# Optimization experiments

Measured on AMD Instinct MI355X. Metric: run time of the kernel, lower is better.

## Reference

```python
import jax, jax.numpy as jnp
import numpy as np

RADIUS = 3
T_STEPS = 2
NEG = -9.0e8
B, L, DEG = 256, 64, 6
FEAT, BOND, FP, OUT = 39, 10, 256, 1


def _leaky(x):
    return jax.nn.leaky_relu(x, 0.01)


def _gru(x, h, wih, whh, bih, bhh):
    # PyTorch GRUCell: gates ordered (r, z, n)
    gi = x @ wih.T + bih
    gh = h @ whh.T + bhh
    ir, iz, inn = jnp.split(gi, 3, axis=-1)
    hr, hz, hn = jnp.split(gh, 3, axis=-1)
    r = jax.nn.sigmoid(ir + hr)
    z = jax.nn.sigmoid(iz + hz)
    n = jnp.tanh(inn + r * hn)
    return (1.0 - z) * n + z * h


def _forward(atom_list, bond_list, atom_mask,
             atom_fc_w, atom_fc_b, neighbor_fc_w, neighbor_fc_b,
             align_w, align_b, attend_w, attend_b,
             gru_wih, gru_whh, gru_bih, gru_bhh,
             mol_align_w, mol_align_b, mol_attend_w, mol_attend_b,
             mol_gru_wih, mol_gru_whh, mol_gru_bih, mol_gru_bhh,
             out_w, out_b,
             atom_degree_list, bond_degree_list):
    b, l, _ = atom_list.shape
    mask = atom_mask[..., None]                                   # [B,L,1]
    atom_feature = _leaky(atom_list @ atom_fc_w.T + atom_fc_b)    # [B,L,FP]

    # per-molecule neighbor gather (padding index = L-1)
    bidx = jnp.arange(b)[:, None, None]
    atom_nb = atom_list[bidx, atom_degree_list]                    # [B,L,deg,FEAT]
    bond_nb = bond_list[bidx, bond_degree_list]                    # [B,L,deg,BOND]
    neighbor_feature = _leaky(
        jnp.concatenate([atom_nb, bond_nb], axis=-1) @ neighbor_fc_w.T + neighbor_fc_b
    )                                                              # [B,L,deg,FP]

    attend_mask = (atom_degree_list != l - 1).astype(atom_feature.dtype)[..., None]
    softmax_mask = jnp.where(atom_degree_list == l - 1, NEG, 0.0).astype(atom_feature.dtype)[..., None]

    for d in range(RADIUS):
        af_exp = jnp.broadcast_to(atom_feature[:, :, None, :], neighbor_feature.shape)
        feature_align = jnp.concatenate([af_exp, neighbor_feature], axis=-1)  # [B,L,deg,2FP]
        align_score = _leaky(feature_align @ align_w[d].T + align_b[d]) + softmax_mask
        attention_weight = jax.nn.softmax(align_score, axis=-2) * attend_mask
        attended = neighbor_feature @ attend_w[d].T + attend_b[d]
        context = jax.nn.elu(jnp.sum(attention_weight * attended, axis=-2))   # [B,L,FP]
        atom_feature = _gru(context.reshape(b * l, -1), atom_feature.reshape(b * l, -1),
                            gru_wih[d], gru_whh[d], gru_bih[d], gru_bhh[d]).reshape(b, l, -1)
        # faithful to original: self-feature broadcast across neighbor dim
        neighbor_feature = jnp.broadcast_to(jax.nn.relu(atom_feature)[:, :, None, :],
                                            neighbor_feature.shape)

    mol_feature = jnp.sum(jax.nn.relu(atom_feature) * mask, axis=-2)          # [B,FP]
    mol_softmax_mask = jnp.where(atom_mask == 0, NEG, 0.0).astype(atom_feature.dtype)[..., None]

    for _ in range(T_STEPS):
        m_exp = jnp.broadcast_to(mol_feature[:, None, :], atom_feature.shape)
        mol_align = jnp.concatenate([m_exp, atom_feature], axis=-1)           # [B,L,2FP]
        mol_score = _leaky(mol_align @ mol_align_w.T + mol_align_b) + mol_softmax_mask
        mol_w = jax.nn.softmax(mol_score, axis=-2) * mask
        attended = atom_feature @ mol_attend_w.T + mol_attend_b
        mol_context = jax.nn.elu(jnp.sum(mol_w * attended, axis=-2))
        mol_feature = _gru(mol_context, mol_feature,
                           mol_gru_wih, mol_gru_whh, mol_gru_bih, mol_gru_bhh)

    mol_prediction = mol_feature @ out_w.T + out_b
    return atom_feature, mol_prediction


def setup_inputs() -> dict:
    key = jax.random.key(0)
    ks = jax.random.split(key, 20)
    s = 0.05
    return {
        "atom_list": jax.random.normal(ks[0], (B, L, FEAT), jnp.float32),
        "bond_list": jax.random.normal(ks[1], (B, L, BOND), jnp.float32),
        "atom_degree_list": jax.random.randint(ks[2], (B, L, DEG), 0, L),
        "bond_degree_list": jax.random.randint(ks[3], (B, L, DEG), 0, L),
        "atom_mask": jnp.ones((B, L), jnp.float32),
        "atom_fc_w": jax.random.normal(ks[4], (FP, FEAT)) * s,
        "atom_fc_b": jnp.zeros((FP,)),
        "neighbor_fc_w": jax.random.normal(ks[5], (FP, FEAT + BOND)) * s,
        "neighbor_fc_b": jnp.zeros((FP,)),
        "align_w": jax.random.normal(ks[6], (RADIUS, 1, 2 * FP)) * s,
        "align_b": jnp.zeros((RADIUS, 1)),
        "attend_w": jax.random.normal(ks[7], (RADIUS, FP, FP)) * s,
        "attend_b": jnp.zeros((RADIUS, FP)),
        "gru_wih": jax.random.normal(ks[8], (RADIUS, 3 * FP, FP)) * s,
        "gru_whh": jax.random.normal(ks[9], (RADIUS, 3 * FP, FP)) * s,
        "gru_bih": jnp.zeros((RADIUS, 3 * FP)),
        "gru_bhh": jnp.zeros((RADIUS, 3 * FP)),
        "mol_align_w": jax.random.normal(ks[10], (1, 2 * FP)) * s,
        "mol_align_b": jnp.zeros((1,)),
        "mol_attend_w": jax.random.normal(ks[11], (FP, FP)) * s,
        "mol_attend_b": jnp.zeros((FP,)),
        "mol_gru_wih": jax.random.normal(ks[12], (3 * FP, FP)) * s,
        "mol_gru_whh": jax.random.normal(ks[13], (3 * FP, FP)) * s,
        "mol_gru_bih": jnp.zeros((3 * FP,)),
        "mol_gru_bhh": jnp.zeros((3 * FP,)),
        "out_w": jax.random.normal(ks[14], (OUT, FP)) * s,
        "out_b": jnp.zeros((OUT,)),
    }


def reference(atom_list, bond_list, atom_degree_list, bond_degree_list, atom_mask,
              atom_fc_w, atom_fc_b, neighbor_fc_w, neighbor_fc_b,
              align_w, align_b, attend_w, attend_b,
              gru_wih, gru_whh, gru_bih, gru_bhh,
              mol_align_w, mol_align_b, mol_attend_w, mol_attend_b,
              mol_gru_wih, mol_gru_whh, mol_gru_bih, mol_gru_bhh,
              out_w, out_b):
    return _forward(atom_list, bond_list, atom_mask,
                    atom_fc_w, atom_fc_b, neighbor_fc_w, neighbor_fc_b,
                    align_w, align_b, attend_w, attend_b,
                    gru_wih, gru_whh, gru_bih, gru_bhh,
                    mol_align_w, mol_align_b, mol_attend_w, mol_attend_b,
                    mol_gru_wih, mol_gru_whh, mol_gru_bih, mol_gru_bhh,
                    out_w, out_b,
                    atom_degree_list, bond_degree_list)
```

## Files before the change

### kernel.cpp

```cpp
#include <hip/hip_runtime.h>
#include <hip/hip_bf16.h>

#define NB 256
#define NL 64
#define DEG 6
#define FEAT 39
#define BOND 10
#define FP 256
#define NEGV (-9.0e8f)

using s16x8 = __attribute__((ext_vector_type(8))) short;
using f32x4 = __attribute__((ext_vector_type(4))) float;

__device__ __forceinline__ unsigned short f2bf(float f){
  unsigned u = __float_as_uint(f);
  u += 0x7fffu + ((u >> 16) & 1u);
  return (unsigned short)(u >> 16);
}
__device__ __forceinline__ float lo16(unsigned u){ return __uint_as_float(u << 16); }
__device__ __forceinline__ float hi16(unsigned u){ return __uint_as_float(u & 0xffff0000u); }

__device__ __forceinline__ float block_sum256(float v, float* scr){
  #pragma unroll
  for(int o=32;o>0;o>>=1) v += __shfl_down(v, o, 64);
  __syncthreads();
  if((threadIdx.x & 63) == 0) scr[threadIdx.x >> 6] = v;
  __syncthreads();
  return scr[0] + scr[1] + scr[2] + scr[3];
}
__device__ __forceinline__ float wave_allsum(float v){
  #pragma unroll
  for(int o=1;o<64;o<<=1) v += __shfl_xor(v, o, 64);
  return v;
}

#define MCVT_N0 65536
#define MCVT_N1 196608
#define MCVT_N2 196608
#define MCVT_TOT (MCVT_N0+MCVT_N1+MCVT_N2)
#define CTXPK_N (3*8*8192)
#define GPK_N   (3*2*8*24576)

__global__ void k_cvt_mol(const float* __restrict__ a0, const float* __restrict__ a1,
                          const float* __restrict__ a2, unsigned short* __restrict__ dst){
  int i = blockIdx.x*256 + threadIdx.x;
  if(i >= MCVT_TOT) return;
  int off = i; const float* src;
  if(off < MCVT_N0) src = a0;
  else { off -= MCVT_N0;
    if(off < MCVT_N1) src = a1;
    else { off -= MCVT_N1; src = a2; } }
  dst[i] = f2bf(src[off]);
}

__global__ void k_pack(const float* __restrict__ attend_w, const float* __restrict__ gru_wih,
                       const float* __restrict__ gru_whh,
                       unsigned short* __restrict__ ctx_pk, unsigned short* __restrict__ gates_pk){
  int i = blockIdx.x*256 + threadIdx.x;
  if(i < CTXPK_N){
    int d = i >> 16;
    int rem = i & 65535;
    int kk = rem >> 13;
    int r2 = rem & 8191;
    int g = r2 >> 9;
    int l = (r2 >> 3) & 63;
    int q = r2 & 7;
    int row = g*16 + (l & 15);
    int k = kk*32 + (l >> 4)*8 + q;
    ctx_pk[i] = f2bf(attend_w[((size_t)d*256 + row)*256 + k]);
  } else {
    int j = i - CTXPK_N;
    if(j >= GPK_N) return;
    int d = j / 393216;
    int rem = j - d*393216;
    int nc = rem / 196608; rem -= nc*196608;
    int kk = rem / 24576;  rem -= kk*24576;
    int f = rem >> 9;
    int l = (rem >> 3) & 63;
    int q = rem & 7;
    int s = f >> 3, g = f & 7;
    int row = nc*128 + g*16 + (l & 15);
    int k = kk*32 + (l >> 4)*8 + q;
    float v = (s < 3) ? gru_wih[(((size_t)d*3 + s)*256 + row)*256 + k]
                      : gru_whh[(((size_t)d*3 + (s-3))*256 + row)*256 + k];
    gates_pk[j] = f2bf(v);
  }
}

__global__ void k_tr(const float* __restrict__ aw, const float* __restrict__ nw,
                     float* __restrict__ afcT, unsigned short* __restrict__ nfcT){
  int i = blockIdx.x*256 + threadIdx.x;
  if(i < 40*256){
    int k = i >> 8, r = i & 255;
    afcT[i] = (k < FEAT) ? aw[r*FEAT + k] : 0.f;
  } else {
    int j = i - 40*256;
    int k = j >> 8, r = j & 255;
    nfcT[j] = (k < FEAT+BOND) ? f2bf(nw[r*(FEAT+BOND) + k]) : (unsigned short)0;
  }
}

__global__ __launch_bounds__(256) void k_atom4(const float* __restrict__ atom,
    const float* __restrict__ afcT, const float* __restrict__ bias, float* __restrict__ af){
  __shared__ float x_s[4][40];
  const int t = threadIdx.x, bl0 = blockIdx.x*4;
  for(int idx=t; idx<4*FEAT; idx+=256){ int a=idx/FEAT, k=idx%FEAT; x_s[a][k]=atom[(bl0+a)*FEAT+k]; }
  if(t < 4) x_s[t][39] = 0.f;
  __syncthreads();
  const int w = t>>6, t0 = (t&63)*4, row = bl0 + w;
  float4 b4 = *(const float4*)&bias[t0];
  float acc[4] = {b4.x, b4.y, b4.z, b4.w};
  for(int k=0;k<40;++k){
    float iv = x_s[w][k];
    float4 wv = *(const float4*)&afcT[(k<<8)+t0];
    acc[0]=fmaf(iv,wv.x,acc[0]); acc[1]=fmaf(iv,wv.y,acc[1]);
    acc[2]=fmaf(iv,wv.z,acc[2]); acc[3]=fmaf(iv,wv.w,acc[3]);
  }
  float4 o;
  o.x = acc[0]>0.f?acc[0]:0.01f*acc[0]; o.y = acc[1]>0.f?acc[1]:0.01f*acc[1];
  o.z = acc[2]>0.f?acc[2]:0.01f*acc[2]; o.w = acc[3]>0.f?acc[3]:0.01f*acc[3];
  *(float4*)&af[(size_t)row*FP + t0] = o;
}

__global__ __launch_bounds__(256) void k_nbr4(const float* __restrict__ atom,
    const float* __restrict__ bond, const int* __restrict__ adl, const int* __restrict__ bdl,
    const unsigned short* __restrict__ nfcT, const float* __restrict__ bn,
    const float* __restrict__ alw, const float* __restrict__ alb,
    const float* __restrict__ af, float* __restrict__ wnf, float* __restrict__ swb){
  __shared__ float in_s[4][DEG][52];
  __shared__ int   ai_s[4][DEG];
  const int t = threadIdx.x, bl0 = blockIdx.x*4;
  if(t < 24){ int a=t/6, d=t%6; ai_s[a][d] = adl[(bl0+a)*DEG + d]; }
  __syncthreads();
  for(int idx=t; idx<4*DEG*(FEAT+BOND); idx+=256){
    int a = idx/(DEG*(FEAT+BOND)), rem = idx%(DEG*(FEAT+BOND));
    int d = rem/(FEAT+BOND), k = rem%(FEAT+BOND);
    int bb = (bl0+a) >> 6;
    float v;
    if(k < FEAT) v = atom[((size_t)bb*NL + ai_s[a][d])*FEAT + k];
    else { int bi = bdl[(bl0+a)*DEG + d]; v = bond[((size_t)bb*NL + bi)*BOND + (k-FEAT)]; }
    in_s[a][d][k] = v;
  }
  if(t < 24){ int a=t/6, d=t%6; in_s[a][d][49]=0.f; in_s[a][d][50]=0.f; in_s[a][d][51]=0.f; }
  __syncthreads();
  const int w = t>>6, lane = t&63, t0 = lane*4, row = bl0 + w;
  float acc[DEG][4] = {};
  for(int k=0;k<52;++k){
    uint2 u = *(const uint2*)&nfcT[(k<<8) + t0];
    float w0=lo16(u.x), w1=hi16(u.x), w2=lo16(u.y), w3=hi16(u.y);
    #pragma unroll
    for(int d=0;d<DEG;++d){
      float iv = in_s[w][d][k];
      acc[d][0]=fmaf(iv,w0,acc[d][0]); acc[d][1]=fmaf(iv,w1,acc[d][1]);
      acc[d][2]=fmaf(iv,w2,acc[d][2]); acc[d][3]=fmaf(iv,w3,acc[d][3]);
    }
  }
  float4 bnv = *(const float4*)&bn[t0];
  float bna[4] = {bnv.x, bnv.y, bnv.z, bnv.w};
  float nf[DEG][4];
  #pragma unroll
  for(int d=0;d<DEG;++d)
    #pragma unroll
    for(int j=0;j<4;++j){ float v = acc[d][j] + bna[j]; nf[d][j] = v>0.f ? v : 0.01f*v; }
  float4 af4 = *(const float4*)&af[(size_t)row*FP + t0];
  float4 a1  = *(const float4*)&alw[t0];
  float4 a2  = *(const float4*)&alw[FP + t0];
  float sa = wave_allsum(af4.x*a1.x + af4.y*a1.y + af4.z*a1.z + af4.w*a1.w);
  float sd[DEG];
  #pragma unroll
  for(int d=0;d<DEG;++d)
    sd[d] = wave_allsum(nf[d][0]*a2.x + nf[d][1]*a2.y + nf[d][2]*a2.z + nf[d][3]*a2.w);
  float ab = alb[0];
  float sc[DEG], msk[DEG];
  #pragma unroll
  for(int d=0;d<DEG;++d){
    float v = sa + sd[d] + ab;
    v = v>0.f ? v : 0.01f*v;
    msk[d] = (ai_s[w][d] == NL-1) ? 0.f : 1.f;
    sc[d] = v + (msk[d] > 0.f ? 0.f : NEGV);
  }
  float m = sc[0];
  #pragma unroll
  for(int d=1;d<DEG;++d) m = fmaxf(m, sc[d]);
  float e[DEG], Z = 0.f;
  #pragma unroll
  for(int d=0;d<DEG;++d){ e[d] = expf(sc[d]-m); Z += e[d]; }
  float wgt[DEG], sw = 0.f;
  #pragma unroll
  for(int d=0;d<DEG;++d){ wgt[d] = e[d]/Z*msk[d]; sw += wgt[d]; }
  float o[4] = {};
  #pragma unroll
  for(int d=0;d<DEG;++d)
    #pragma unroll
    for(int j=0;j<4;++j) o[j] = fmaf(wgt[d], nf[d][j], o[j]);
  float4 ov; ov.x=o[0]; ov.y=o[1]; ov.z=o[2]; ov.w=o[3];
  *(float4*)&wnf[(size_t)row*FP + t0] = ov;
  if(lane == 0) swb[row] = sw;
}

__global__ __launch_bounds__(512) void k_radius4(
    const float* __restrict__ wnf, float* __restrict__ af, const float* __restrict__ swb,
    const unsigned short* __restrict__ ctx_pk, const unsigned short* __restrict__ gates_pk,
    const float* __restrict__ attend_b,
    const float* __restrict__ gru_bih, const float* __restrict__ gru_bhh){
  __shared__ __align__(16) unsigned short Cf[32*512];
  const int t = threadIdx.x;
  const int w = t>>6, lane = t&63, lr = lane&15, ks = lane>>4;
  const int wm = w>>2, wn = w&3;
  const int m0 = blockIdx.x*64;

  for(int d=0; d<3; ++d){
    const float* bat  = attend_b + d*256;
    const float* bihd = gru_bih + d*768;
    const float* bhhd = gru_bhh + d*768;

    __syncthreads();
    f32x4 acc2[2][4] = {};
    #pragma unroll
    for(int kk=0; kk<8; ++kk){
      const unsigned short* ct = ctx_pk + ((size_t)d*8 + kk)*8192;
      s16x8 xf[2];
      #pragma unroll
      for(int mf=0; mf<2; ++mf){
        int row = m0 + wm*32 + mf*16 + lr;
        float4 v0, v1;
        if(d == 0){
          const float* sp = wnf + (size_t)row*256 + kk*32 + ks*8;
          v0 = *(const float4*)sp; v1 = *(const float4*)(sp+4);
        } else {
          const float* sp = af + (size_t)row*256 + kk*32 + ks*8;
          v0 = *(const float4*)sp; v1 = *(const float4*)(sp+4);
          float sw = swb[row];
          v0.x=fmaxf(v0.x,0.f)*sw; v0.y=fmaxf(v0.y,0.f)*sw;
          v0.z=fmaxf(v0.z,0.f)*sw; v0.w=fmaxf(v0.w,0.f)*sw;
          v1.x=fmaxf(v1.x,0.f)*sw; v1.y=fmaxf(v1.y,0.f)*sw;
          v1.z=fmaxf(v1.z,0.f)*sw; v1.w=fmaxf(v1.w,0.f)*sw;
        }
        unsigned short tmp[8] = {f2bf(v0.x),f2bf(v0.y),f2bf(v0.z),f2bf(v0.w),
                                 f2bf(v1.x),f2bf(v1.y),f2bf(v1.z),f2bf(v1.w)};
        xf[mf] = *(s16x8*)tmp;
      }
      #pragma unroll
      for(int nf=0; nf<4; ++nf){
        s16x8 wf = *(const s16x8*)(ct + ((wn*4 + nf)*64 + lane)*8);
        acc2[0][nf] = __builtin_amdgcn_mfma_f32_16x16x32_bf16(wf, xf[0], acc2[0][nf],0,0,0);
        acc2[1][nf] = __builtin_amdgcn_mfma_f32_16x16x32_bf16(wf, xf[1], acc2[1][nf],0,0,0);
      }
    }
    #pragma unroll
    for(int mf=0; mf<2; ++mf){
      float swv = swb[m0 + wm*32 + mf*16 + lr];
      #pragma unroll
      for(int nf=0; nf<4; ++nf){
        int nb = wn*64 + nf*16 + ks*4;
        float4 b4 = *(const float4*)&bat[nb];
        float bj[4] = {b4.x, b4.y, b4.z, b4.w};
        unsigned short o4[4];
        #pragma unroll
        for(int j=0;j<4;++j){
          float v = acc2[mf][nf][j] + swv*bj[j];
          v = v > 0.f ? v : expm1f(v);
          o4[j] = f2bf(v);
        }
        int gm = wm*2 + mf;
        int kkp = wn*2 + (nf>>1);
        int lhi = ((nf & 1) << 1) | (ks >> 1);
        int addr = (gm*8 + kkp)*512 + (lhi*16 + lr)*8 + (ks & 1)*4;
        *(uint2*)&Cf[addr] = *(uint2*)o4;
      }
    }
    __syncthreads();
    float hnew0[2][2][4];
    float hnew1[2][2][4];
    for(int nc=0; nc<2; ++nc){
      f32x4 aR[2][2] = {}, aZ[2][2] = {}, aN[2][2] = {}, aH[2][2] = {};
      #pragma unroll
      for(int kk=0; kk<8; ++kk){
        const unsigned short* gp = gates_pk + ((size_t)(d*2 + nc)*8 + kk)*24576;
        s16x8 hf[2];
        #pragma unroll
        for(int mf=0; mf<2; ++mf){
          int row = m0 + wm*32 + mf*16 + lr;
          const float* sp = af + (size_t)row*256 + kk*32 + ks*8;
          float4 v0 = *(const float4*)sp, v1 = *(const float4*)(sp+4);
          unsigned short tmp[8] = {f2bf(v0.x),f2bf(v0.y),f2bf(v0.z),f2bf(v0.w),
                                   f2bf(v1.x),f2bf(v1.y),f2bf(v1.z),f2bf(v1.w)};
          hf[mf] = *(s16x8*)tmp;
        }
        s16x8 cf0 = *(const s16x8*)&Cf[((wm*2 + 0)*8 + kk)*512 + lane*8];
        s16x8 cf1 = *(const s16x8*)&Cf[((wm*2 + 1)*8 + kk)*512 + lane*8];
        #pragma unroll
        for(int fn=0; fn<2; ++fn){
          int g = wn*2 + fn;
          s16x8 b0 = *(const s16x8*)(gp + ((0*8 + g)*64 + lane)*8);
          s16x8 b1 = *(const s16x8*)(gp + ((1*8 + g)*64 + lane)*8);
          s16x8 b2 = *(const s16x8*)(gp + ((2*8 + g)*64 + lane)*8);
          s16x8 b3 = *(const s16x8*)(gp + ((3*8 + g)*64 + lane)*8);
          s16x8 b4 = *(const s16x8*)(gp + ((4*8 + g)*64 + lane)*8);
          s16x8 b5 = *(const s16x8*)(gp + ((5*8 + g)*64 + lane)*8);
          aR[0][fn] = __builtin_amdgcn_mfma_f32_16x16x32_bf16(cf0, b0, aR[0][fn],0,0,0);
          aR[1][fn] = __builtin_amdgcn_mfma_f32_16x16x32_bf16(cf1, b0, aR[1][fn],0,0,0);
          aZ[0][fn] = __builtin_amdgcn_mfma_f32_16x16x32_bf16(cf0, b1, aZ[0][fn],0,0,0);
          aZ[1][fn] = __builtin_amdgcn_mfma_f32_16x16x32_bf16(cf1, b1, aZ[1][fn],0,0,0);
          aN[0][fn] = __builtin_amdgcn_mfma_f32_16x16x32_bf16(cf0, b2, aN[0][fn],0,0,0);
          aN[1][fn] = __builtin_amdgcn_mfma_f32_16x16x32_bf16(cf1, b2, aN[1][fn],0,0,0);
          aR[0][fn] = __builtin_amdgcn_mfma_f32_16x16x32_bf16(hf[0], b3, aR[0][fn],0,0,0);
          aR[1][fn] = __builtin_amdgcn_mfma_f32_16x16x32_bf16(hf[1], b3, aR[1][fn],0,0,0);
          aZ[0][fn] = __builtin_amdgcn_mfma_f32_16x16x32_bf16(hf[0], b4, aZ[0][fn],0,0,0);
          aZ[1][fn] = __builtin_amdgcn_mfma_f32_16x16x32_bf16(hf[1], b4, aZ[1][fn],0,0,0);
          aH[0][fn] = __builtin_amdgcn_mfma_f32_16x16x32_bf16(hf[0], b5, aH[0][fn],0,0,0);
          aH[1][fn] = __builtin_amdgcn_mfma_f32_16x16x32_bf16(hf[1], b5, aH[1][fn],0,0,0);
        }
      }
      float (*hn_)[2][4] = (nc == 0) ? hnew0 : hnew1;
      int nbase = nc*128;
      #pragma unroll
      for(int mf=0; mf<2; ++mf)
        #pragma unroll
        for(int fn=0; fn<2; ++fn){
          int n = nbase + wn*32 + fn*16 + lr;
          float brz = bihd[n] + bhhd[n];
          float bzz = bihd[256+n] + bhhd[256+n];
          float bnn = bihd[512+n];
          float bhn = bhhd[512+n];
          #pragma unroll
          for(int j=0;j<4;++j){
            int m = m0 + wm*32 + mf*16 + ks*4 + j;
            float hold = af[(size_t)m*256 + n];
            float r = 1.f/(1.f + expf(-(aR[mf][fn][j] + brz)));
            float z = 1.f/(1.f + expf(-(aZ[mf][fn][j] + bzz)));
            float ng = tanhf(aN[mf][fn][j] + bnn + r*(aH[mf][fn][j] + bhn));
            hn_[mf][fn][j] = (1.f - z)*ng + z*hold;
          }
        }
    }
    __syncthreads();
    #pragma unroll
    for(int nc=0; nc<2; ++nc){
      float (*hn_)[2][4] = (nc == 0) ? hnew0 : hnew1;
      int nbase = nc*128;
      #pragma unroll
      for(int mf=0; mf<2; ++mf)
        #pragma unroll
        for(int fn=0; fn<2; ++fn){
          int n = nbase + wn*32 + fn*16 + lr;
          #pragma unroll
          for(int j=0;j<4;++j){
            int m = m0 + wm*32 + mf*16 + ks*4 + j;
            af[(size_t)m*256 + n] = hn_[mf][fn][j];
          }
        }
    }
  }
}

__global__ __launch_bounds__(256) void k_lin_gemm(
    const float* __restrict__ Xsrc, const unsigned short* __restrict__ Wbf,
    const float* __restrict__ bias, float* __restrict__ Y){
  __shared__ unsigned short A_lds[64][264];
  __shared__ unsigned short B_lds[64][264];
  const int t = threadIdx.x;
  const int m0 = (blockIdx.x >> 2) * 64, n0 = (blockIdx.x & 3) * 64;
  const int rb = t >> 4, cb = (t & 15) * 16;
  for(int i=0;i<4;++i){
    int row = i*16 + rb;
    const float* src = Xsrc + (size_t)(m0+row)*FP + cb;
    unsigned short tmp[16];
    #pragma unroll
    for(int q=0;q<4;++q){
      float4 v = ((const float4*)src)[q];
      tmp[q*4+0]=f2bf(v.x); tmp[q*4+1]=f2bf(v.y); tmp[q*4+2]=f2bf(v.z); tmp[q*4+3]=f2bf(v.w);
    }
    *(s16x8*)&A_lds[row][cb]   = *(s16x8*)&tmp[0];
    *(s16x8*)&A_lds[row][cb+8] = *(s16x8*)&tmp[8];
    const unsigned short* wsrc = Wbf + (size_t)(n0+row)*FP + cb;
    *(s16x8*)&B_lds[row][cb]   = *(const s16x8*)&wsrc[0];
    *(s16x8*)&B_lds[row][cb+8] = *(const s16x8*)&wsrc[8];
  }
  __syncthreads();
  const int w = t>>6, lane = t&63, lr = lane&15, ks = lane>>4;
  const int wr = (w>>1)*32, wc = (w&1)*32;
  f32x4 acc[2][2] = {};
  #pragma unroll
  for(int kk=0;kk<8;++kk){
    int ko = kk*32 + ks*8;
    s16x8 a0 = *(const s16x8*)&A_lds[wr+lr][ko];
    s16x8 a1 = *(const s16x8*)&A_lds[wr+16+lr][ko];
    s16x8 b0 = *(const s16x8*)&B_lds[wc+lr][ko];
    s16x8 b1 = *(const s16x8*)&B_lds[wc+16+lr][ko];
    acc[0][0] = __builtin_amdgcn_mfma_f32_16x16x32_bf16(a0,b0,acc[0][0],0,0,0);
    acc[0][1] = __builtin_amdgcn_mfma_f32_16x16x32_bf16(a0,b1,acc[0][1],0,0,0);
    acc[1][0] = __builtin_amdgcn_mfma_f32_16x16x32_bf16(a1,b0,acc[1][0],0,0,0);
    acc[1][1] = __builtin_amdgcn_mfma_f32_16x16x32_bf16(a1,b1,acc[1][1],0,0,0);
  }
  #pragma unroll
  for(int fm=0;fm<2;++fm)
    #pragma unroll
    for(int fn=0;fn<2;++fn){
      int n = n0 + wc + fn*16 + lr;
      float bv = bias[n];
      #pragma unroll
      for(int j=0;j<4;++j){
        int m = m0 + wr + fm*16 + ks*4 + j;
        Y[(size_t)m*FP + n] = acc[fm][fn][j] + bv;
      }
    }
}

__global__ __launch_bounds__(256) void k_gates32(
    const unsigned short* __restrict__ ctxbf, const float* __restrict__ h_glob,
    const unsigned short* __restrict__ wihbf, const unsigned short* __restrict__ whhbf,
    const float* __restrict__ bih, const float* __restrict__ bhh,
    float* __restrict__ h_out){
  __shared__ unsigned short A_ctx[32][40];
  __shared__ unsigned short A_h[32][40];
  __shared__ unsigned short B_lds[6][64][40];
  const int t = threadIdx.x;
  const int m0 = (blockIdx.x >> 2) * 32, nc = (blockIdx.x & 3) * 64;
  const int w = t>>6, lane = t&63, lr = lane&15, ks = lane>>4;
  const int mh = (w>>1)*16, nh = (w&1)*32;
  f32x4 acc[6][2] = {};
  for(int kk=0;kk<8;++kk){
    const int k0 = kk*32;
    __syncthreads();
    {
      int row = t>>3, c4 = (t&7)*4;
      *(uint2*)&A_ctx[row][c4] = *(const uint2*)(ctxbf + (size_t)(m0+row)*FP + k0 + c4);
      float4 hv = *(const float4*)(h_glob + (size_t)(m0+row)*FP + k0 + c4);
      unsigned short ht[4] = {f2bf(hv.x), f2bf(hv.y), f2bf(hv.z), f2bf(hv.w)};
      *(uint2*)&A_h[row][c4] = *(uint2*)ht;
    }
    #pragma unroll
    for(int i=0;i<6;++i){
      int idx = i*256 + t;
      int s = idx >> 8, rem = idx & 255;
      int row = rem >> 2, c8 = (rem & 3)*8;
      const unsigned short* wsrc = (s < 3)
          ? wihbf + (size_t)(s*FP + nc + row)*FP + k0 + c8
          : whhbf + (size_t)((s-3)*FP + nc + row)*FP + k0 + c8;
      *(s16x8*)&B_lds[s][row][c8] = *(const s16x8*)wsrc;
    }
    __syncthreads();
    s16x8 ac = *(const s16x8*)&A_ctx[mh+lr][ks*8];
    s16x8 ah = *(const s16x8*)&A_h[mh+lr][ks*8];
    #pragma unroll
    for(int s=0;s<6;++s){
      s16x8 a = (s < 3) ? ac : ah;
      #pragma unroll
      for(int fn=0;fn<2;++fn){
        s16x8 b = *(const s16x8*)&B_lds[s][nh+fn*16+lr][ks*8];
        acc[s][fn] = __builtin_amdgcn_mfma_f32_16x16x32_bf16(a,b,acc[s][fn],0,0,0);
      }
    }
  }
  #pragma unroll
  for(int fn=0;fn<2;++fn){
    int n = nc + nh + fn*16 + lr;
    float bir = bih[n], biz = bih[FP+n], bin_ = bih[2*FP+n];
    float bhr = bhh[n], bhz = bhh[FP+n], bhn  = bhh[2*FP+n];
    #pragma unroll
    for(int j=0;j<4;++j){
      int m = m0 + mh + ks*4 + j;
      float h = h_glob[(size_t)m*FP + n];
      float ir = acc[0][fn][j]+bir, iz = acc[1][fn][j]+biz, inn = acc[2][fn][j]+bin_;
      float hr = acc[3][fn][j]+bhr, hz = acc[4][fn][j]+bhz, hn  = acc[5][fn][j]+bhn;
      float r = 1.f/(1.f + expf(-(ir+hr)));
      float z = 1.f/(1.f + expf(-(iz+hz)));
      float ng = tanhf(inn + r*hn);
      h_out[(size_t)m*FP + n] = (1.f-z)*ng + z*h;
    }
  }
}

__global__ void k_finalize(const float* __restrict__ af, const float* __restrict__ mask,
                           float* __restrict__ molfeat, float* __restrict__ out_af){
  const int b = blockIdx.x, t = threadIdx.x;
  __shared__ float msk_s[NL];
  if(t < NL) msk_s[t] = mask[b*NL + t];
  __syncthreads();
  float mf = 0.f;
  for(int l=0;l<NL;++l){
    float v = af[(size_t)(b*NL + l)*FP + t];
    out_af[(size_t)(b*NL + l)*FP + t] = v;
    mf = fmaf(fmaxf(v,0.f), msk_s[l], mf);
  }
  molfeat[b*FP + t] = mf;
}

__global__ void k_mol_ctx(const float* __restrict__ af, const float* __restrict__ att,
    const float* __restrict__ mfin, const float* __restrict__ maw,
    const float* __restrict__ mabp, const float* __restrict__ mask,
    unsigned short* __restrict__ ctxb){
  const int b = blockIdx.x, t = threadIdx.x;
  __shared__ float mf_s[FP];
  __shared__ float sc_s[NL], aw_s[NL], scr[4];
  mf_s[t] = mfin[b*FP + t];
  __syncthreads();
  float sa = block_sum256(maw[t]*mf_s[t], scr);
  int l = t >> 2, q = t & 3;
  float p = 0.f;
  {
    const float4* ar = (const float4*)(af + (size_t)(b*NL + l)*FP + q*64);
    const float4* w2 = (const float4*)(maw + FP + q*64);
    #pragma unroll
    for(int k=0;k<16;++k){
      float4 a = ar[k], ww = w2[k];
      p = fmaf(a.x,ww.x,p); p = fmaf(a.y,ww.y,p);
      p = fmaf(a.z,ww.z,p); p = fmaf(a.w,ww.w,p);
    }
  }
  p += __shfl_xor(p, 1, 64);
  p += __shfl_xor(p, 2, 64);
  if(q == 0){
    float mv = mask[b*NL + l];
    float v = sa + p + mabp[0];
    v = v > 0.f ? v : 0.01f*v;
    sc_s[l] = v + (mv == 0.f ? NEGV : 0.f);
  }
  __syncthreads();
  if(t < NL){
    float s = sc_s[t];
    float m = s;
    #pragma unroll
    for(int o=32;o>0;o>>=1) m = fmaxf(m, __shfl_xor(m, o, 64));
    float e = expf(s - m);
    float Z = e;
    #pragma unroll
    for(int o=32;o>0;o>>=1) Z += __shfl_xor(Z, o, 64);
    aw_s[t] = e / Z * mask[b*NL + t];
  }
  __syncthreads();
  float acc = 0.f;
  for(int l2=0;l2<NL;++l2) acc = fmaf(aw_s[l2], att[(size_t)(b*NL + l2)*FP + t], acc);
  float c = acc > 0.f ? acc : expm1f(acc);
  ctxb[b*FP + t] = f2bf(c);
}

__global__ void k_out(const float* __restrict__ molfeat, const float* __restrict__ ow,
                      const float* __restrict__ ob, float* __restrict__ outp){
  const int b = blockIdx.x, t = threadIdx.x;
  __shared__ float scr[4];
  float s = block_sum256(molfeat[b*FP + t]*ow[t], scr);
  if(t == 0) outp[b] = s + ob[0];
}

extern "C" void kernel_launch(void* const* d_in, const int* in_sizes, int n_in,
                              void* d_out, int out_size, void* d_ws, size_t ws_size,
                              hipStream_t stream){
  const float* atom_list = (const float*)d_in[0];
  const float* bond_list = (const float*)d_in[1];
  const int*   adl       = (const int*)d_in[2];
  const int*   bdl       = (const int*)d_in[3];
  const float* amask     = (const float*)d_in[4];
  const float* afc_w     = (const float*)d_in[5];
  const float* afc_b     = (const float*)d_in[6];
  const float* nfc_w     = (const float*)d_in[7];
  const float* nfc_b     = (const float*)d_in[8];
  const float* align_w   = (const float*)d_in[9];
  const float* align_b   = (const float*)d_in[10];
  const float* attend_w  = (const float*)d_in[11];
  const float* attend_b  = (const float*)d_in[12];
  const float* gru_wih   = (const float*)d_in[13];
  const float* gru_whh   = (const float*)d_in[14];
  const float* gru_bih   = (const float*)d_in[15];
  const float* gru_bhh   = (const float*)d_in[16];
  const float* mol_align_w  = (const float*)d_in[17];
  const float* mol_align_b  = (const float*)d_in[18];
  const float* mol_attend_w = (const float*)d_in[19];
  const float* mol_attend_b = (const float*)d_in[20];
  const float* mg_wih    = (const float*)d_in[21];
  const float* mg_whh    = (const float*)d_in[22];
  const float* mg_bih    = (const float*)d_in[23];
  const float* mg_bhh    = (const float*)d_in[24];
  const float* out_w     = (const float*)d_in[25];
  const float* out_b     = (const float*)d_in[26];

  float* out_af   = (float*)d_out;
  float* out_pred = out_af + (size_t)NB*NL*FP;

  const size_t NROW = (size_t)NB*NL;
  const size_t F32_CNT = 2*NROW*FP + NROW + 2*(size_t)NB*FP + 40*256;
  const size_t U16_CNT = (size_t)NB*FP + MCVT_TOT + 52*256 + CTXPK_N + GPK_N;
  const size_t NEED = F32_CNT*4 + U16_CNT*2;

  if(ws_size >= NEED){
    float* af_a    = (float*)d_ws;
    float* wnf     = af_a + NROW*FP;
    float* swb     = wnf  + NROW*FP;
    float* mf_a    = swb  + NROW;
    float* mf_b    = mf_a + (size_t)NB*FP;
    float* afcT    = mf_b + (size_t)NB*FP;
    unsigned short* ctxbf_m = (unsigned short*)(afcT + 40*256);
    unsigned short* maw_bf  = ctxbf_m + (size_t)NB*FP;
    unsigned short* mgih_bf = maw_bf + MCVT_N0;
    unsigned short* mghh_bf = mgih_bf + MCVT_N1;
    unsigned short* nfcT_bf = mghh_bf + MCVT_N2;
    unsigned short* ctx_pk  = nfcT_bf + 52*256;
    unsigned short* gates_pk= ctx_pk + CTXPK_N;

    k_cvt_mol<<<(MCVT_TOT+255)/256, 256, 0, stream>>>(mol_attend_w, mg_wih, mg_whh, maw_bf);
    k_pack<<<(CTXPK_N+GPK_N)/256, 256, 0, stream>>>(attend_w, gru_wih, gru_whh, ctx_pk, gates_pk);
    k_tr<<<(40*256 + 52*256)/256, 256, 0, stream>>>(afc_w, nfc_w, afcT, nfcT_bf);

    k_atom4<<<NB*NL/4, 256, 0, stream>>>(atom_list, afcT, afc_b, af_a);
    k_nbr4<<<NB*NL/4, 256, 0, stream>>>(atom_list, bond_list, adl, bdl,
                                        nfcT_bf, nfc_b, align_w, align_b, af_a, wnf, swb);
    k_radius4<<<NB*NL/64, 512, 0, stream>>>(wnf, af_a, swb, ctx_pk, gates_pk,
                                            attend_b, gru_bih, gru_bhh);
    k_lin_gemm<<<(NB*NL/64)*4, 256, 0, stream>>>(af_a, maw_bf, mol_attend_b, wnf);
    k_finalize<<<NB, 256, 0, stream>>>(af_a, amask, mf_a, out_af);
    float* m_cur = mf_a; float* m_nxt = mf_b;
    for(int s=0; s<2; ++s){
      k_mol_ctx<<<NB, 256, 0, stream>>>(af_a, wnf, m_cur, mol_align_w, mol_align_b,
                                        amask, ctxbf_m);
      k_gates32<<<(NB/32)*4, 256, 0, stream>>>(ctxbf_m, m_cur, mgih_bf, mghh_bf,
                                               mg_bih, mg_bhh, m_nxt);
      float* tmp = m_cur; m_cur = m_nxt; m_nxt = tmp;
    }
    k_out<<<NB, 256, 0, stream>>>(m_cur, out_w, out_b, out_pred);
  } else {
    float* af = (float*)d_ws;
    k_atom4<<<NB*NL/4, 256, 0, stream>>>(atom_list, (const float*)afc_w, afc_b, af);
    (void)bond_list; (void)adl; (void)bdl; (void)amask;
    (void)align_w; (void)align_b; (void)attend_w; (void)attend_b;
    (void)gru_wih; (void)gru_whh; (void)gru_bih; (void)gru_bhh;
    (void)mol_align_w; (void)mol_align_b; (void)mol_attend_w; (void)mol_attend_b;
    (void)mg_wih; (void)mg_whh; (void)mg_bih; (void)mg_bhh; (void)out_w; (void)out_b;
  }
}
```

Baseline: 367.9 us.

## Stage radius weights through double-buffered LDS with register prefetch, halve row tile

The radius kernel now streams the attend and GRU weight tiles through a double-buffered shared-memory ring, prefetching the next tile into registers while the current one feeds the MFMAs. Previously every wave read its weights directly from global memory. The row tile per block shrinks from 64 to 32 and the GRU weight packing is re-laid out into 64-column chunks, so twice as many blocks launch with a min-blocks launch bound. This should hide weight-load latency and raise occupancy, at the cost of a barrier on every k-step and each block re-reading the full weight set for fewer rows.

```diff
diff --git a/kernel.cpp b/kernel.cpp
--- a/kernel.cpp
+++ b/kernel.cpp
@@ -38,8 +38,10 @@
 #define MCVT_N1 196608
 #define MCVT_N2 196608
 #define MCVT_TOT (MCVT_N0+MCVT_N1+MCVT_N2)
-#define CTXPK_N (3*8*8192)
-#define GPK_N   (3*2*8*24576)
+#define CT_U16 8192
+#define GT_U16 12288
+#define CTXPK_N (3*8*CT_U16)
+#define GPK_N   (3*4*8*GT_U16)
 
 __global__ void k_cvt_mol(const float* __restrict__ a0, const float* __restrict__ a1,
                           const float* __restrict__ a2, unsigned short* __restrict__ dst){
@@ -73,13 +75,13 @@
     if(j >= GPK_N) return;
     int d = j / 393216;
     int rem = j - d*393216;
-    int nc = rem / 196608; rem -= nc*196608;
-    int kk = rem / 24576;  rem -= kk*24576;
+    int nc = rem / 98304;  rem -= nc*98304;
+    int kk = rem / 12288;  rem -= kk*12288;
     int f = rem >> 9;
     int l = (rem >> 3) & 63;
     int q = rem & 7;
-    int s = f >> 3, g = f & 7;
-    int row = nc*128 + g*16 + (l & 15);
+    int s = f >> 2, gl = f & 3;
+    int row = nc*64 + gl*16 + (l & 15);
     int k = kk*32 + (l >> 4)*8 + q;
     float v = (s < 3) ? gru_wih[(((size_t)d*3 + s)*256 + row)*256 + k]
                       : gru_whh[(((size_t)d*3 + (s-3))*256 + row)*256 + k];
@@ -198,158 +200,148 @@
   if(lane == 0) swb[row] = sw;
 }
 
-__global__ __launch_bounds__(512) void k_radius4(
+__global__ __launch_bounds__(512, 4) void k_radius6(
     const float* __restrict__ wnf, float* __restrict__ af, const float* __restrict__ swb,
     const unsigned short* __restrict__ ctx_pk, const unsigned short* __restrict__ gates_pk,
     const float* __restrict__ attend_b,
     const float* __restrict__ gru_bih, const float* __restrict__ gru_bhh){
-  __shared__ __align__(16) unsigned short Cf[32*512];
+  __shared__ __align__(16) unsigned short Cf[2*8*512];
+  __shared__ __align__(16) unsigned short Bu[2][GT_U16];
   const int t = threadIdx.x;
   const int w = t>>6, lane = t&63, lr = lane&15, ks = lane>>4;
   const int wm = w>>2, wn = w&3;
-  const int m0 = blockIdx.x*64;
+  const int m0 = blockIdx.x*32;
+
+  s16x8 pf[3]; int pfn = 0;
+  auto LOADS = [&](int s){
+    if(s >= 120) return;
+    int d2 = s/40, r = s - d2*40;
+    const unsigned short* src; int n;
+    if(r < 8){ n = 2; src = ctx_pk + ((size_t)d2*8 + r)*CT_U16; }
+    else { int g = r - 8; n = 3; src = gates_pk + ((size_t)(d2*4 + (g>>3))*8 + (g&7))*GT_U16; }
+    pfn = n;
+    #pragma unroll
+    for(int c=0;c<3;++c) if(c < n) pf[c] = *(const s16x8*)(src + (w + c*8)*512 + lane*8);
+  };
+  auto WRITET = [&](int h){
+    #pragma unroll
+    for(int c=0;c<3;++c) if(c < pfn) *(s16x8*)&Bu[h][(w + c*8)*512 + lane*8] = pf[c];
+  };
+
+  LOADS(0);
+  WRITET(0);
+  LOADS(1);
+  int half = 0;
+  const float swv = swb[m0 + wm*16 + lr];
 
   for(int d=0; d<3; ++d){
     const float* bat  = attend_b + d*256;
     const float* bihd = gru_bih + d*768;
     const float* bhhd = gru_bhh + d*768;
-
-    __syncthreads();
-    f32x4 acc2[2][4] = {};
-    #pragma unroll
+    f32x4 acc2[4] = {};
     for(int kk=0; kk<8; ++kk){
-      const unsigned short* ct = ctx_pk + ((size_t)d*8 + kk)*8192;
-      s16x8 xf[2];
+      int s = d*40 + kk;
+      __syncthreads();
+      WRITET(half^1);
+      LOADS(s+2);
+      int row = m0 + wm*16 + lr;
+      float4 v0, v1;
+      if(d == 0){
+        const float* sp = wnf + (size_t)row*256 + kk*32 + ks*8;
+        v0 = *(const float4*)sp; v1 = *(const float4*)(sp+4);
+      } else {
+        const float* sp = af + (size_t)row*256 + kk*32 + ks*8;
+        v0 = *(const float4*)sp; v1 = *(const float4*)(sp+4);
+        v0.x=fmaxf(v0.x,0.f)*swv; v0.y=fmaxf(v0.y,0.f)*swv;
+        v0.z=fmaxf(v0.z,0.f)*swv; v0.w=fmaxf(v0.w,0.f)*swv;
+        v1.x=fmaxf(v1.x,0.f)*swv; v1.y=fmaxf(v1.y,0.f)*swv;
+        v1.z=fmaxf(v1.z,0.f)*swv; v1.w=fmaxf(v1.w,0.f)*swv;
+      }
+      unsigned short tmp[8] = {f2bf(v0.x),f2bf(v0.y),f2bf(v0.z),f2bf(v0.w),
+                               f2bf(v1.x),f2bf(v1.y),f2bf(v1.z),f2bf(v1.w)};
+      s16x8 xf = *(s16x8*)tmp;
       #pragma unroll
-      for(int mf=0; mf<2; ++mf){
-        int row = m0 + wm*32 + mf*16 + lr;
-        float4 v0, v1;
-        if(d == 0){
-          const float* sp = wnf + (size_t)row*256 + kk*32 + ks*8;
-          v0 = *(const float4*)sp; v1 = *(const float4*)(sp+4);
-        } else {
-          const float* sp = af + (size_t)row*256 + kk*32 + ks*8;
-          v0 = *(const float4*)sp; v1 = *(const float4*)(sp+4);
-          float sw = swb[row];
-          v0.x=fmaxf(v0.x,0.f)*sw; v0.y=fmaxf(v0.y,0.f)*sw;
-          v0.z=fmaxf(v0.z,0.f)*sw; v0.w=fmaxf(v0.w,0.f)*sw;
-          v1.x=fmaxf(v1.x,0.f)*sw; v1.y=fmaxf(v1.y,0.f)*sw;
-          v1.z=fmaxf(v1.z,0.f)*sw; v1.w=fmaxf(v1.w,0.f)*sw;
-        }
+      for(int nf=0; nf<4; ++nf){
+        s16x8 wf = *(const s16x8*)&Bu[half][((wn*4 + nf)*64 + lane)*8];
+        acc2[nf] = __builtin_amdgcn_mfma_f32_16x16x32_bf16(wf, xf, acc2[nf],0,0,0);
+      }
+      half ^= 1;
+    }
+    #pragma unroll
+    for(int nf=0; nf<4; ++nf){
+      int nb = wn*64 + nf*16 + ks*4;
+      float4 b4 = *(const float4*)&bat[nb];
+      float bj[4] = {b4.x, b4.y, b4.z, b4.w};
+      unsigned short o4[4];
+      #pragma unroll
+      for(int j=0;j<4;++j){
+        float v = acc2[nf][j] + swv*bj[j];
+        v = v > 0.f ? v : expm1f(v);
+        o4[j] = f2bf(v);
+      }
+      int gm = wm;
+      int kkp = wn*2 + (nf>>1);
+      int lhi = ((nf & 1) << 1) | (ks >> 1);
+      int addr = (gm*8 + kkp)*512 + (lhi*16 + lr)*8 + (ks & 1)*4;
+      *(uint2*)&Cf[addr] = *(uint2*)o4;
+    }
+    float hnew[4][4];
+    #pragma unroll
+    for(int nc=0; nc<4; ++nc){
+      f32x4 aR = {}, aZ = {}, aN = {}, aH = {};
+      #pragma unroll
+      for(int kk=0; kk<8; ++kk){
+        int s = d*40 + 8 + nc*8 + kk;
+        __syncthreads();
+        if(s < 119) WRITET(half^1);
+        LOADS(s+2);
+        int row = m0 + wm*16 + lr;
+        const float* sp = af + (size_t)row*256 + kk*32 + ks*8;
+        float4 v0 = *(const float4*)sp, v1 = *(const float4*)(sp+4);
         unsigned short tmp[8] = {f2bf(v0.x),f2bf(v0.y),f2bf(v0.z),f2bf(v0.w),
                                  f2bf(v1.x),f2bf(v1.y),f2bf(v1.z),f2bf(v1.w)};
-        xf[mf] = *(s16x8*)tmp;
-      }
-      #pragma unroll
-      for(int nf=0; nf<4; ++nf){
-        s16x8 wf = *(const s16x8*)(ct + ((wn*4 + nf)*64 + lane)*8);
-        acc2[0][nf] = __builtin_amdgcn_mfma_f32_16x16x32_bf16(wf, xf[0], acc2[0][nf],0,0,0);
-        acc2[1][nf] = __builtin_amdgcn_mfma_f32_16x16x32_bf16(wf, xf[1], acc2[1][nf],0,0,0);
-      }
-    }
-    #pragma unroll
-    for(int mf=0; mf<2; ++mf){
-      float swv = swb[m0 + wm*32 + mf*16 + lr];
-      #pragma unroll
-      for(int nf=0; nf<4; ++nf){
-        int nb = wn*64 + nf*16 + ks*4;
-        float4 b4 = *(const float4*)&bat[nb];
-        float bj[4] = {b4.x, b4.y, b4.z, b4.w};
-        unsigned short o4[4];
+        s16x8 hf = *(s16x8*)tmp;
+        s16x8 cf = *(const s16x8*)&Cf[(wm*8 + kk)*512 + lane*8];
+        s16x8 b0 = *(const s16x8*)&Bu[half][((0*4 + wn)*64 + lane)*8];
+        s16x8 b1 = *(const s16x8*)&Bu[half][((1*4 + wn)*64 + lane)*8];
+        s16x8 b2 = *(const s16x8*)&Bu[half][((2*4 + wn)*64 + lane)*8];
+        s16x8 b3 = *(const s16x8*)&Bu[half][((3*4 + wn)*64 + lane)*8];
+        s16x8 b4 = *(const s16x8*)&Bu[half][((4*4 + wn)*64 + lane)*8];
+        s16x8 b5 = *(const s16x8*)&Bu[half][((5*4 + wn)*64 + lane)*8];
+        aR = __builtin_amdgcn_mfma_f32_16x16x32_bf16(cf, b0, aR,0,0,0);
+        aZ = __builtin_amdgcn_mfma_f32_16x16x32_bf16(cf, b1, aZ,0,0,0);
+        aN = __builtin_amdgcn_mfma_f32_16x16x32_bf16(cf, b2, aN,0,0,0);
+        aR = __builtin_amdgcn_mfma_f32_16x16x32_bf16(hf, b3, aR,0,0,0);
+        aZ = __builtin_amdgcn_mfma_f32_16x16x32_bf16(hf, b4, aZ,0,0,0);
+        aH = __builtin_amdgcn_mfma_f32_16x16x32_bf16(hf, b5, aH,0,0,0);
+        half ^= 1;
+      }
+      {
+        int n = nc*64 + wn*16 + lr;
+        float brz = bihd[n] + bhhd[n];
+        float bzz = bihd[256+n] + bhhd[256+n];
+        float bnn = bihd[512+n];
+        float bhn = bhhd[512+n];
         #pragma unroll
         for(int j=0;j<4;++j){
-          float v = acc2[mf][nf][j] + swv*bj[j];
-          v = v > 0.f ? v : expm1f(v);
-          o4[j] = f2bf(v);
+          int m = m0 + wm*16 + ks*4 + j;
+          float hold = af[(size_t)m*256 + n];
+          float r = 1.f/(1.f + expf(-(aR[j] + brz)));
+          float z = 1.f/(1.f + expf(-(aZ[j] + bzz)));
+          float ng = tanhf(aN[j] + bnn + r*(aH[j] + bhn));
+          hnew[nc][j] = (1.f - z)*ng + z*hold;
         }
-        int gm = wm*2 + mf;
-        int kkp = wn*2 + (nf>>1);
-        int lhi = ((nf & 1) << 1) | (ks >> 1);
-        int addr = (gm*8 + kkp)*512 + (lhi*16 + lr)*8 + (ks & 1)*4;
-        *(uint2*)&Cf[addr] = *(uint2*)o4;
       }
     }
     __syncthreads();
-    float hnew0[2][2][4];
-    float hnew1[2][2][4];
-    for(int nc=0; nc<2; ++nc){
-      f32x4 aR[2][2] = {}, aZ[2][2] = {}, aN[2][2] = {}, aH[2][2] = {};
+    #pragma unroll
+    for(int nc=0; nc<4; ++nc){
+      int n = nc*64 + wn*16 + lr;
       #pragma unroll
-      for(int kk=0; kk<8; ++kk){
-        const unsigned short* gp = gates_pk + ((size_t)(d*2 + nc)*8 + kk)*24576;
-        s16x8 hf[2];
-        #pragma unroll
-        for(int mf=0; mf<2; ++mf){
-          int row = m0 + wm*32 + mf*16 + lr;
-          const float* sp = af + (size_t)row*256 + kk*32 + ks*8;
-          float4 v0 = *(const float4*)sp, v1 = *(const float4*)(sp+4);
-          unsigned short tmp[8] = {f2bf(v0.x),f2bf(v0.y),f2bf(v0.z),f2bf(v0.w),
-                                   f2bf(v1.x),f2bf(v1.y),f2bf(v1.z),f2bf(v1.w)};
-          hf[mf] = *(s16x8*)tmp;
-        }
-        s16x8 cf0 = *(const s16x8*)&Cf[((wm*2 + 0)*8 + kk)*512 + lane*8];
-        s16x8 cf1 = *(const s16x8*)&Cf[((wm*2 + 1)*8 + kk)*512 + lane*8];
-        #pragma unroll
-        for(int fn=0; fn<2; ++fn){
-          int g = wn*2 + fn;
-          s16x8 b0 = *(const s16x8*)(gp + ((0*8 + g)*64 + lane)*8);
-          s16x8 b1 = *(const s16x8*)(gp + ((1*8 + g)*64 + lane)*8);
-          s16x8 b2 = *(const s16x8*)(gp + ((2*8 + g)*64 + lane)*8);
-          s16x8 b3 = *(const s16x8*)(gp + ((3*8 + g)*64 + lane)*8);
-          s16x8 b4 = *(const s16x8*)(gp + ((4*8 + g)*64 + lane)*8);
-          s16x8 b5 = *(const s16x8*)(gp + ((5*8 + g)*64 + lane)*8);
-          aR[0][fn] = __builtin_amdgcn_mfma_f32_16x16x32_bf16(cf0, b0, aR[0][fn],0,0,0);
-          aR[1][fn] = __builtin_amdgcn_mfma_f32_16x16x32_bf16(cf1, b0, aR[1][fn],0,0,0);
-          aZ[0][fn] = __builtin_amdgcn_mfma_f32_16x16x32_bf16(cf0, b1, aZ[0][fn],0,0,0);
-          aZ[1][fn] = __builtin_amdgcn_mfma_f32_16x16x32_bf16(cf1, b1, aZ[1][fn],0,0,0);
-          aN[0][fn] = __builtin_amdgcn_mfma_f32_16x16x32_bf16(cf0, b2, aN[0][fn],0,0,0);
-          aN[1][fn] = __builtin_amdgcn_mfma_f32_16x16x32_bf16(cf1, b2, aN[1][fn],0,0,0);
-          aR[0][fn] = __builtin_amdgcn_mfma_f32_16x16x32_bf16(hf[0], b3, aR[0][fn],0,0,0);
-          aR[1][fn] = __builtin_amdgcn_mfma_f32_16x16x32_bf16(hf[1], b3, aR[1][fn],0,0,0);
-          aZ[0][fn] = __builtin_amdgcn_mfma_f32_16x16x32_bf16(hf[0], b4, aZ[0][fn],0,0,0);
-          aZ[1][fn] = __builtin_amdgcn_mfma_f32_16x16x32_bf16(hf[1], b4, aZ[1][fn],0,0,0);
-          aH[0][fn] = __builtin_amdgcn_mfma_f32_16x16x32_bf16(hf[0], b5, aH[0][fn],0,0,0);
-          aH[1][fn] = __builtin_amdgcn_mfma_f32_16x16x32_bf16(hf[1], b5, aH[1][fn],0,0,0);
-        }
-      }
-      float (*hn_)[2][4] = (nc == 0) ? hnew0 : hnew1;
-      int nbase = nc*128;
-      #pragma unroll
-      for(int mf=0; mf<2; ++mf)
-        #pragma unroll
-        for(int fn=0; fn<2; ++fn){
-          int n = nbase + wn*32 + fn*16 + lr;
-          float brz = bihd[n] + bhhd[n];
-          float bzz = bihd[256+n] + bhhd[256+n];
-          float bnn = bihd[512+n];
-          float bhn = bhhd[512+n];
-          #pragma unroll
-          for(int j=0;j<4;++j){
-            int m = m0 + wm*32 + mf*16 + ks*4 + j;
-            float hold = af[(size_t)m*256 + n];
-            float r = 1.f/(1.f + expf(-(aR[mf][fn][j] + brz)));
-            float z = 1.f/(1.f + expf(-(aZ[mf][fn][j] + bzz)));
-            float ng = tanhf(aN[mf][fn][j] + bnn + r*(aH[mf][fn][j] + bhn));
-            hn_[mf][fn][j] = (1.f - z)*ng + z*hold;
-          }
-        }
-    }
-    __syncthreads();
-    #pragma unroll
-    for(int nc=0; nc<2; ++nc){
-      float (*hn_)[2][4] = (nc == 0) ? hnew0 : hnew1;
-      int nbase = nc*128;
-      #pragma unroll
-      for(int mf=0; mf<2; ++mf)
-        #pragma unroll
-        for(int fn=0; fn<2; ++fn){
-          int n = nbase + wn*32 + fn*16 + lr;
-          #pragma unroll
-          for(int j=0;j<4;++j){
-            int m = m0 + wm*32 + mf*16 + ks*4 + j;
-            af[(size_t)m*256 + n] = hn_[mf][fn][j];
-          }
-        }
+      for(int j=0;j<4;++j){
+        int m = m0 + wm*16 + ks*4 + j;
+        af[(size_t)m*256 + n] = hnew[nc][j];
+      }
     }
   }
 }
@@ -605,7 +597,7 @@
     k_atom4<<<NB*NL/4, 256, 0, stream>>>(atom_list, afcT, afc_b, af_a);
     k_nbr4<<<NB*NL/4, 256, 0, stream>>>(atom_list, bond_list, adl, bdl,
                                         nfcT_bf, nfc_b, align_w, align_b, af_a, wnf, swb);
-    k_radius4<<<NB*NL/64, 512, 0, stream>>>(wnf, af_a, swb, ctx_pk, gates_pk,
+    k_radius6<<<NB*NL/32, 512, 0, stream>>>(wnf, af_a, swb, ctx_pk, gates_pk,
                                             attend_b, gru_bih, gru_bhh);
     k_lin_gemm<<<(NB*NL/64)*4, 256, 0, stream>>>(af_a, maw_bf, mol_attend_b, wnf);
     k_finalize<<<NB, 256, 0, stream>>>(af_a, amask, mf_a, out_af);
```

Result: slower. 382.3 us (+3.9%).
